# Performance work log

Measured on AMD Instinct MI355X. Metric: run time of the kernel, lower is better.

The kernel has to match this reference:

```python
import jax, jax.numpy as jnp
import numpy as np


def _shift(x, k):
    # roll time axis forward by k, zero-filling the first k steps
    if k == 0:
        return x
    return jnp.pad(x, ((0, 0), (k, 0), (0, 0)))[:, : x.shape[1]]


def _stu_conv(u, v, n):
    # u: (B,L,D), v: (L,K) spectral filters; non-tensordot branch of conv()
    B, L, D = u.shape
    K = v.shape[1]
    sgn = jnp.where(jnp.arange(L) % 2 == 1, -1.0, 1.0).astype(jnp.float32)[None, :, None, None]
    ue = jnp.broadcast_to(u[:, :, None, :], (B, L, K, D)).astype(jnp.float32)
    U = jnp.stack([ue, ue * sgn], axis=-1)                     # (B,L,K,D,2)
    Uf = jnp.fft.rfft(U, n=n, axis=1)
    vf = jnp.fft.rfft(v.astype(jnp.float32)[None, :, :, None, None], n=n, axis=1)
    Uc = jnp.fft.irfft(vf * Uf, n=n, axis=1)[:, :L]            # (B,L,K,D,2)
    U_plus = Uc[..., 0]
    U_minus = Uc[..., 1] * sgn
    return U_plus.astype(u.dtype), U_minus.astype(u.dtype)


def setup_inputs() -> dict:
    key = jax.random.key(0)
    ks = jax.random.split(key, 6)
    B, L, D, K, k_u, k_y = 2, 1024, 512, 16, 3, 2
    u = jax.random.normal(ks[0], (B, L, D), jnp.float32)
    filters = jax.random.normal(ks[1], (L, K), jnp.float32) / np.float32(np.sqrt(L))
    M_u = jax.random.normal(ks[2], (D, k_u, D), jnp.float32) * 0.01
    M_y = jax.random.normal(ks[3], (D, k_y, D), jnp.float32) * 0.01
    M_phi_plus = jax.random.normal(ks[4], (K, D, D), jnp.float32) * 0.01
    M_phi_minus = jax.random.normal(ks[5], (K, D, D), jnp.float32) * 0.01
    return {"u": u, "filters": filters, "M_u": M_u, "M_y": M_y,
            "M_phi_plus": M_phi_plus, "M_phi_minus": M_phi_minus}


def reference(u, filters, M_u, M_y, M_phi_plus, M_phi_minus):
    B, L, D = u.shape
    n = 1 << int(np.ceil(np.log2(2 * L - 1)))  # nearest power of two >= 2L-1
    k_u = M_u.shape[1]
    k_y = M_y.shape[1]

    # FFT-based long convolution with the +/- sign trick
    U_plus, U_minus = _stu_conv(u, filters, n)
    spectral = (jnp.einsum('blkd,kdo->blo', U_plus, M_phi_plus)
                + jnp.einsum('blkd,kdo->blo', U_minus, M_phi_minus))

    # input-AR term of compute_ar_strict: sum_j u[t+1-j] @ M_u[:, j-1].T (shifts 0..k_u-1)
    u_sh = jnp.stack([_shift(u, j - 1) for j in range(1, k_u + 1)], axis=1)  # (B,k_u,L,D)
    y_in = jnp.einsum('bjlf,ijf->bli', u_sh, M_u)

    z = spectral + y_in  # (B,L,D)

    # output-AR recurrence of compute_ar_strict as a scan
    def step(y_buf, z_t):
        y_t = z_t + jnp.einsum('bjf,djf->bd', y_buf, M_y)
        y_buf = jnp.concatenate([y_t[:, None], y_buf[:, :-1]], axis=1)
        return y_buf, y_t

    _, ys = jax.lax.scan(step, jnp.zeros((B, k_y, D), z.dtype), jnp.swapaxes(z, 0, 1))
    return jnp.swapaxes(ys, 0, 1)  # (B,L,D)
```

## Files before the change

### kernel.cpp

```cpp
#include <hip/hip_runtime.h>
#include <hip/hip_bf16.h>


using bf16 = __hip_bfloat16;
typedef __attribute__((ext_vector_type(8))) short bf16x8;
typedef __attribute__((ext_vector_type(4))) float f32x4;

#define B_   2
#define L_   1024
#define D_   512
#define K_   16
#define KT   17920
#define ROWS 2048
#define NTAP 6
#define PBLD 3584
#define SPLITD 14
#define SPLITR 6
#define ZBROWS 1032
#define NKS 40
#define NTD 20

#define WAIT_VM6 0x0F76
#define WAIT_VM4 0x0F74
#define WAIT_VM0 0x0F70

__device__ __forceinline__ void gll16(const void* g, void* l) {
    __builtin_amdgcn_global_load_lds(
        (const __attribute__((address_space(1))) unsigned int*)g,
        (__attribute__((address_space(3))) unsigned int*)l, 16, 0, 0);
}

__global__ void prep_all(const float* __restrict__ u, const float* __restrict__ fil,
                         const float* __restrict__ Mu, const float* __restrict__ My,
                         const float* __restrict__ Mp, const float* __restrict__ Mm,
                         bf16* __restrict__ U, bf16* __restrict__ BT,
                         bf16* __restrict__ PB, bf16* __restrict__ W,
                         bf16* __restrict__ Myb, bf16* __restrict__ BTT,
                         bf16* __restrict__ uPT) {
    __shared__ bf16 t[64][72];
    int bid = blockIdx.x, tid = threadIdx.x;
    auto pack4 = [](float4 v) {
        ushort4 o; bf16 h;
        h = __float2bfloat16(v.x); o.x = *(unsigned short*)&h;
        h = __float2bfloat16(v.y); o.y = *(unsigned short*)&h;
        h = __float2bfloat16(v.z); o.z = *(unsigned short*)&h;
        h = __float2bfloat16(v.w); o.w = *(unsigned short*)&h;
        return o;
    };
    if (bid < 3072) {
        int e4 = bid * 256 + tid;
        int r = e4 / 384, rem = e4 % 384;
        int tt = rem >> 7, f = (rem & 127) * 4;
        int b = r >> 10, l = r & 1023;
        float4 v = {0.f, 0.f, 0.f, 0.f};
        if (l >= tt) v = *(const float4*)&u[((size_t)b * L_ + l - tt) * D_ + f];
        *(ushort4*)&U[(size_t)r * KT + 16384 + tt * 512 + f] = pack4(v);
    } else if (bid < 3840) {
        int e4 = (bid - 3072) * 256 + tid;
        int o = e4 / 384, tf4 = (e4 % 384) * 4;
        float4 v = *(const float4*)&Mu[(size_t)o * 1536 + tf4];
        *(ushort4*)&BT[(size_t)o * KT + 16384 + tf4] = pack4(v);
    } else if (bid < 4352) {
        int e4 = (bid - 3840) * 256 + tid;
        int n = e4 >> 8, c4 = (e4 & 255) * 4;
        float4 v;
        if (c4 < 512) {
            v.x = (n == c4) ? 1.f : 0.f;     v.y = (n == c4 + 1) ? 1.f : 0.f;
            v.z = (n == c4 + 2) ? 1.f : 0.f; v.w = (n == c4 + 3) ? 1.f : 0.f;
        } else v = *(const float4*)&My[(size_t)n * 1024 + (c4 - 512)];
        *(ushort4*)&PB[(size_t)n * PBLD + c4] = pack4(v);
    } else if (bid < 5120) {
        int tile = bid - 4352;
        int set = tile >> 8, rem = tile & 255;
        int k = rem >> 4, g = (rem >> 2) & 3, kb = rem & 3;
        for (int idx = tid; idx < 4096; idx += 256) {
            int i = idx >> 5, jp = idx & 31;
            int j = ((jp >> 3) ^ ((i >> 1) & 3)) * 8 + (jp & 7);
            int x = g * 128 + i - kb * 32 - j - (set == 2 ? 1 : 0);
            float v = 0.f;
            if (x >= 0) {
                int row = (set == 0) ? 2 * x : 2 * x + 1;
                v = fil[row * K_ + k];
            }
            W[(size_t)tile * 4096 + idx] = __float2bfloat16(v);
        }
    } else if (bid < 5632) {
        int e4 = (bid - 5120) * 256 + tid;
        float4 v = *(const float4*)&My[(size_t)e4 * 4];
        *(ushort4*)&Myb[(size_t)e4 * 4] = pack4(v);
    } else {
        int tt = bid - 5632;
        int zb = tt >> 6, rem = tt & 63;
        int bx = rem & 7, by = rem >> 3;
        int col = tid & 63, r0 = (tid >> 6) * 16;
        if (zb < 32) {
            int dt = bx * 64, ot = by * 64, c = zb;
            int k = c & 15;
            const float* sp = Mp + (size_t)k * D_ * D_;
            const float* sm = Mm + (size_t)k * D_ * D_;
            float sg = (c < 16) ? 1.f : -1.f;
            for (int i = 0; i < 16; ++i) {
                size_t o_ = (size_t)(dt + r0 + i) * D_ + ot + col;
                t[r0 + i][col] = __float2bfloat16(sp[o_] + sg * sm[o_]);
            }
            __syncthreads();
            for (int i = 0; i < 16; ++i)
                BT[(size_t)(ot + r0 + i) * KT + c * D_ + dt + col] = t[col][r0 + i];
        } else if (zb < 34) {
            int h = zb - 32;
            int dt = bx * 64, ft = by * 64;
            for (int i = 0; i < 16; ++i)
                t[r0 + i][col] = __float2bfloat16(My[(size_t)(dt + r0 + i) * 1024 + (1 - h) * 512 + ft + col]);
            __syncthreads();
            for (int i = 0; i < 16; ++i)
                BTT[(size_t)(ft + r0 + i) * 1024 + h * 512 + dt + col] = t[col][r0 + i];
        } else {
            for (int it = 0; it < 4; ++it) {
                int b = it >> 1, p = it & 1;
                int mt = bx * 64, dt = by * 64;
                __syncthreads();
                for (int i = 0; i < 16; ++i)
                    t[r0 + i][col] = __float2bfloat16(u[((size_t)b * L_ + 2 * (mt + r0 + i) + p) * D_ + dt + col]);
                __syncthreads();
                for (int i = 0; i < 16; ++i)
                    uPT[((size_t)it * 512 + dt + r0 + i) * 512 + mt + col] = t[col][r0 + i];
            }
        }
    }
}

__device__ __forceinline__ void phi_body(
    const bf16* A, int lda, const bf16* BT, int ldb,
    bf16* out, int ldo, int klen, const bf16* add, int lad,
    int row0, int col0, bf16* sA, bf16* sB)
{
    const int tid = threadIdx.x, lane = tid & 63, wave = tid >> 6;
    const int wm = (wave & 1) * 64, wn = (wave >> 1) * 64;
    const int ml = lane & 15, q = lane >> 4;
    const int srow = lane >> 2, scol = (((lane & 3) ^ ((srow >> 1) & 3))) * 8;
    const int swz = ((ml >> 1) & 3);
    f32x4 acc[4][4] = {};

    for (int k = 0; k < klen; k += 32) {
        __syncthreads();
        #pragma unroll
        for (int repi = 0; repi < 2; ++repi) {
            int a = wave + repi * 4;
            gll16(A  + (size_t)(row0 + a * 16 + srow) * lda + k + scol, &sA[a * 512]);
            gll16(BT + (size_t)(col0 + a * 16 + srow) * ldb + k + scol, &sB[a * 512]);
        }
        __syncthreads();
        bf16x8 af[4], bfr[4];
        #pragma unroll
        for (int i = 0; i < 4; ++i)
            af[i] = *(const bf16x8*)&sA[(wm + i * 16 + ml) * 32 + (q ^ swz) * 8];
        #pragma unroll
        for (int j = 0; j < 4; ++j)
            bfr[j] = *(const bf16x8*)&sB[(wn + j * 16 + ml) * 32 + (q ^ swz) * 8];
        #pragma unroll
        for (int i = 0; i < 4; ++i)
            #pragma unroll
            for (int j = 0; j < 4; ++j)
                acc[i][j] = __builtin_amdgcn_mfma_f32_16x16x32_bf16(af[i], bfr[j], acc[i][j], 0, 0, 0);
    }
    #pragma unroll
    for (int i = 0; i < 4; ++i)
        #pragma unroll
        for (int j = 0; j < 4; ++j)
            #pragma unroll
            for (int reg = 0; reg < 4; ++reg) {
                int r = row0 + wm + i * 16 + q * 4 + reg;
                int cc = col0 + wn + j * 16 + ml;
                float v = acc[i][j][reg];
                if (add) v += __bfloat162float(add[(size_t)r * lad + cc]);
                out[(size_t)r * ldo + cc] = __float2bfloat16(v);
            }
}

__global__ void k_ztaps(const bf16* __restrict__ partD, float* __restrict__ z,
                        bf16* __restrict__ zbuf, bf16* PB, const bf16* BTT) {
    __shared__ bf16 sA[4096];
    __shared__ bf16 sB[4096];
    int bid = blockIdx.x;
    if (bid < 32) {
        int row0 = (bid & 3) * 128, col0 = (bid >> 2) * 128;
        phi_body(PB + 3 * 512, PBLD, BTT, 1024, PB + 5 * 512, PBLD, 1024,
                 nullptr, 0, row0, col0, sA, sB);
        return;
    }
    if (bid == 32) {
        ushort4 z4 = {0, 0, 0, 0};
        for (int i = 0; i < 8; ++i) {
            int e4 = i * 256 + threadIdx.x;
            int b = e4 >> 10, rem = e4 & 1023;
            int g = rem >> 7, c4 = (rem & 127) * 4;
            *(ushort4*)&zbuf[(size_t)(b * ZBROWS + g) * 512 + c4] = z4;
        }
        return;
    }
    int t = (bid - 33) * 256 + threadIdx.x;
    int r = t >> 7, f4 = (t & 127) * 4;
    const ushort4* p = (const ushort4*)partD;
    float4 s = {0.f, 0.f, 0.f, 0.f};
    #pragma unroll
    for (int c = 0; c < SPLITD; ++c) {
        ushort4 v = p[(size_t)c * (ROWS * D_ / 4) + t];
        s.x += __uint_as_float((unsigned)v.x << 16);
        s.y += __uint_as_float((unsigned)v.y << 16);
        s.z += __uint_as_float((unsigned)v.z << 16);
        s.w += __uint_as_float((unsigned)v.w << 16);
    }
    ((float4*)z)[t] = s;
    ushort4 zb4;
    { bf16 h;
      h = __float2bfloat16(s.x); zb4.x = *(unsigned short*)&h;
      h = __float2bfloat16(s.y); zb4.y = *(unsigned short*)&h;
      h = __float2bfloat16(s.z); zb4.z = *(unsigned short*)&h;
      h = __float2bfloat16(s.w); zb4.w = *(unsigned short*)&h; }
    int b = r >> 10, li = r & 1023;
    *(ushort4*)&zbuf[(size_t)(b * ZBROWS + 8 + li) * 512 + f4] = zb4;
}

__global__ void reduce_out(const float* __restrict__ z, const bf16* __restrict__ partR,
                           float* __restrict__ out) {
    int t = blockIdx.x * 256 + threadIdx.x;
    if (t >= ROWS * D_ / 4) return;
    float4 s = ((const float4*)z)[t];
    const ushort4* p = (const ushort4*)partR;
    #pragma unroll
    for (int c = 0; c < SPLITR; ++c) {
        ushort4 v = p[(size_t)c * (ROWS * D_ / 4) + t];
        s.x += __uint_as_float((unsigned)v.x << 16);
        s.y += __uint_as_float((unsigned)v.y << 16);
        s.z += __uint_as_float((unsigned)v.z << 16);
        s.w += __uint_as_float((unsigned)v.w << 16);
    }
    ((float4*)out)[t] = s;
}

__global__ __launch_bounds__(256, 3) void conv_misc(
    const bf16* __restrict__ W, const bf16* __restrict__ uPT,
    bf16* __restrict__ U,
    const bf16* PB, const bf16* BTT, const bf16* Myb)
{
    __shared__ bf16 sA[3][4096];
    __shared__ bf16 sB[3][4096];
    const int z = blockIdx.z;
    if (z < 3) {
        int row0 = blockIdx.x * 128, col0 = blockIdx.y * 128;
        bf16* BTTw = (bf16*)BTT; bf16* PBw = (bf16*)PB;
        if (z == 0)
            phi_body(PB, PBLD, BTT, 1024, PBw + 2 * 512, PBLD, 1024,
                     nullptr, 0, row0, col0, &sA[0][0], &sB[0][0]);
        else if (z == 1)
            phi_body(BTT + 512, 1024, Myb + 512, 1024,
                     BTTw + (size_t)512 * 1024, 1024, 512,
                     nullptr, 0, row0, col0, &sA[0][0], &sB[0][0]);
        else
            phi_body(BTT + 512, 1024, Myb, 1024,
                     BTTw + (size_t)512 * 1024 + 512, 1024, 512,
                     BTT, 1024, row0, col0, &sA[0][0], &sB[0][0]);
        return;
    }
    const int zc = z - 3;
    const int mt = 3 - blockIdx.x, dt = blockIdx.y * 128;
    const int t = zc & 3, b = (zc >> 2) & 1, k = zc >> 3;
    const int pb_ = t & 1;
    const int p = (t & 1) ^ (t >> 1);
    const int set = (t < 2) ? 0 : (t == 2 ? 1 : 2);
    const int ch = (t < 2) ? k : 16 + k;
    const int plane = b * 2 + pb_;
    const int tid = threadIdx.x, lane = tid & 63, wave = tid >> 6;
    const int wm = (wave & 1) * 64, wn = (wave >> 1) * 64;
    const int ml = lane & 15, q = lane >> 4;
    const int srow = lane >> 2, scol = (((lane & 3) ^ ((srow >> 1) & 3))) * 8;
    const int swz = ((ml >> 1) & 3);
    f32x4 acc[4][4] = {};
    const int n = (mt + 1) * 4;

    const bf16* bB0 = uPT + ((size_t)plane * 512 + dt + wave * 16       + srow) * 512 + scol;
    const bf16* bB1 = uPT + ((size_t)plane * 512 + dt + (wave + 4) * 16 + srow) * 512 + scol;
    const bf16* wbase = W + ((size_t)(set * 16 + k) * 16) * 4096;
    auto stage = [&](int s, int buf) {
        const bf16* wt = wbase + ((size_t)((mt - (s >> 2)) * 4 + (s & 3))) * 4096;
        gll16(wt + wave * 512 + lane * 8, &sA[buf][wave * 512]);
        gll16(wt + (wave + 4) * 512 + lane * 8, &sA[buf][(wave + 4) * 512]);
        gll16(bB0 + s * 32, &sB[buf][wave * 512]);
        gll16(bB1 + s * 32, &sB[buf][(wave + 4) * 512]);
    };
    auto compute = [&](int c) {
        bf16x8 af[4], bfr[4];
        #pragma unroll
        for (int i = 0; i < 4; ++i)
            af[i] = *(const bf16x8*)&sA[c][(wm + i * 16 + ml) * 32 + (q ^ swz) * 8];
        #pragma unroll
        for (int j = 0; j < 4; ++j)
            bfr[j] = *(const bf16x8*)&sB[c][(wn + j * 16 + ml) * 32 + (q ^ swz) * 8];
        #pragma unroll
        for (int i = 0; i < 4; ++i)
            #pragma unroll
            for (int j = 0; j < 4; ++j)
                acc[i][j] = __builtin_amdgcn_mfma_f32_16x16x32_bf16(af[i], bfr[j], acc[i][j], 0, 0, 0);
    };
    stage(0, 0); stage(1, 1);
    int c = 0, nb = 2;
    for (int i = 0; i < n - 1; ++i) {
        __builtin_amdgcn_s_waitcnt(WAIT_VM4);
        __builtin_amdgcn_s_barrier();
        if (i + 2 < n) stage(i + 2, nb);
        compute(c);
        c = (c == 2) ? 0 : c + 1; nb = (nb == 2) ? 0 : nb + 1;
    }
    __builtin_amdgcn_s_waitcnt(WAIT_VM0);
    __builtin_amdgcn_s_barrier();
    compute(c);

    #pragma unroll
    for (int i = 0; i < 4; ++i)
        #pragma unroll
        for (int j = 0; j < 4; ++j)
            #pragma unroll
            for (int reg = 0; reg < 4; ++reg) {
                int m = mt * 128 + wm + i * 16 + q * 4 + reg;
                int l = 2 * m + p;
                int d = dt + wn + j * 16 + ml;
                U[(size_t)(b * L_ + l) * KT + ch * 512 + d] = __float2bfloat16(acc[i][j][reg]);
            }
}

__global__ __launch_bounds__(512, 2) void gemm_d(
    const bf16* __restrict__ U, const bf16* __restrict__ BT,
    bf16* __restrict__ part, const bf16* PB, const bf16* BTT)
{
    __shared__ bf16 sA[4][8192];
    __shared__ bf16 sB[4][8192];
    int id = blockIdx.x;
    const int tid = threadIdx.x, lane = tid & 63, wave = tid >> 6;
    if (id < 32) {
        if (wave >= 4) {
            for (int i = 0; i < 64; ++i) __syncthreads();
            return;
        }
        int r0_ = (id & 3) * 128, c0_ = (id >> 2) * 128;
        phi_body(PB + 512, PBLD, BTT, 1024, (bf16*)PB + 3 * 512, PBLD, 1024,
                 nullptr, 0, r0_, c0_, &sA[0][0], &sB[0][0]);
        return;
    }
    id -= 32;
    const int zz = id >> 4;
    const int n_ = id & 15;
    const int row0 = (n_ >> 1) * 256, col0 = (n_ & 1) * 256;
    const int k0 = zz * (KT / SPLITD);

    const int wm = (wave >> 2) * 128;
    const int wn = (wave & 3) * 64;
    const int ml = lane & 15, q16 = lane >> 4;
    const int srow = lane >> 2, scol = (((lane & 3) ^ ((srow >> 1) & 3))) * 8;
    const int swz = ((ml >> 1) & 3);
    const int koff = (q16 ^ swz) * 8;

    const int a0 = 2 * wave, a1 = 2 * wave + 1;
    const bf16* bA0 = U  + (size_t)(row0 + a0 * 16 + srow) * KT + k0 + scol;
    const bf16* bA1 = U  + (size_t)(row0 + a1 * 16 + srow) * KT + k0 + scol;
    const bf16* bB0 = BT + (size_t)(col0 + a0 * 16 + srow) * KT + k0 + scol;
    const bf16* bB1 = BT + (size_t)(col0 + a1 * 16 + srow) * KT + k0 + scol;
    auto stageA = [&](int s) {
        if (s >= NKS) return;
        gll16(bA0 + s * 32, &sA[s & 3][a0 * 512]);
        gll16(bA1 + s * 32, &sA[s & 3][a1 * 512]);
    };
    auto stageB = [&](int s) {
        if (s >= NKS) return;
        gll16(bB0 + s * 32, &sB[s & 3][a0 * 512]);
        gll16(bB1 + s * 32, &sB[s & 3][a1 * 512]);
    };

    f32x4 acc[8][4] = {};

    stageB(0); stageB(1); stageA(0); stageA(1);
    stageB(2); stageB(3); stageA(2);
    __builtin_amdgcn_s_waitcnt(WAIT_VM6);
    __builtin_amdgcn_s_barrier();

    for (int t = 0; t < NTD; ++t) {
        const int u0 = (2 * t) & 3, u1 = u0 + 1;
        bf16x8 bfr[4][2];
        #pragma unroll
        for (int ph = 0; ph < 4; ++ph) {
            bf16x8 af[2][2];
            if (ph == 0) {
                #pragma unroll
                for (int fc = 0; fc < 4; ++fc) {
                    bfr[fc][0] = *(const bf16x8*)&sB[u0][(wn + fc * 16 + ml) * 32 + koff];
                    bfr[fc][1] = *(const bf16x8*)&sB[u1][(wn + fc * 16 + ml) * 32 + koff];
                }
            }
            #pragma unroll
            for (int f2 = 0; f2 < 2; ++f2) {
                int R = wm + (2 * ph + f2) * 16 + ml;
                af[f2][0] = *(const bf16x8*)&sA[u0][R * 32 + koff];
                af[f2][1] = *(const bf16x8*)&sA[u1][R * 32 + koff];
            }
            if (ph == 0)      stageA(2 * t + 3);
            else if (ph == 1) stageB(2 * t + 4);
            else if (ph == 2) stageB(2 * t + 5);
            else              stageA(2 * t + 4);
            __builtin_amdgcn_s_barrier();
            __builtin_amdgcn_s_setprio(1);
            #pragma unroll
            for (int f2 = 0; f2 < 2; ++f2)
                #pragma unroll
                for (int fc = 0; fc < 4; ++fc) {
                    acc[2 * ph + f2][fc] = __builtin_amdgcn_mfma_f32_16x16x32_bf16(
                        af[f2][0], bfr[fc][0], acc[2 * ph + f2][fc], 0, 0, 0);
                    acc[2 * ph + f2][fc] = __builtin_amdgcn_mfma_f32_16x16x32_bf16(
                        af[f2][1], bfr[fc][1], acc[2 * ph + f2][fc], 0, 0, 0);
                }
            __builtin_amdgcn_s_setprio(0);
            if (ph == 3) {
                if (t < NTD - 2)       __builtin_amdgcn_s_waitcnt(WAIT_VM6);
                else if (t == NTD - 2) __builtin_amdgcn_s_waitcnt(WAIT_VM0);
            }
            __builtin_amdgcn_s_barrier();
        }
    }

    bf16* o = part + (size_t)zz * ROWS * D_;
    #pragma unroll
    for (int i = 0; i < 8; ++i)
        #pragma unroll
        for (int j = 0; j < 4; ++j)
            #pragma unroll
            for (int reg = 0; reg < 4; ++reg) {
                int r = row0 + wm + i * 16 + q16 * 4 + reg;
                int cc = col0 + wn + j * 16 + ml;
                o[(size_t)r * D_ + cc] = __float2bfloat16(acc[i][j][reg]);
            }
}

__device__ __forceinline__ void mm128_pair(
    const bf16* Abase, int alda, const bf16* Bbase, int ldb, int n,
    bf16* o, int row0, int col0, bf16 (*sA)[4096], bf16 (*sB)[4096])
{
    const int tid = threadIdx.x, lane = tid & 63, wave = tid >> 6;
    const int wm = (wave & 1) * 64, wn = (wave >> 1) * 64;
    const int ml = lane & 15, q = lane >> 4;
    const int srow = lane >> 2, scol = (((lane & 3) ^ ((srow >> 1) & 3))) * 8;
    const int swz = ((ml >> 1) & 3);
    f32x4 acc[4][4] = {};

    const bf16* bA0 = Abase + (size_t)(wave * 16 + srow) * alda + scol;
    const bf16* bA1 = Abase + (size_t)((wave + 4) * 16 + srow) * alda + scol;
    const bf16* bB0 = Bbase + (size_t)(wave * 16 + srow) * ldb + scol;
    const bf16* bB1 = Bbase + (size_t)((wave + 4) * 16 + srow) * ldb + scol;
    auto stage = [&](int s) {
        int buf = s & 3;
        gll16(bA0 + s * 32, &sA[buf][wave * 512]);
        gll16(bA1 + s * 32, &sA[buf][(wave + 4) * 512]);
        gll16(bB0 + s * 32, &sB[buf][wave * 512]);
        gll16(bB1 + s * 32, &sB[buf][(wave + 4) * 512]);
    };
    auto compute = [&](int c) {
        bf16x8 af[4], bfr[4];
        #pragma unroll
        for (int i = 0; i < 4; ++i)
            af[i] = *(const bf16x8*)&sA[c][(wm + i * 16 + ml) * 32 + (q ^ swz) * 8];
        #pragma unroll
        for (int j = 0; j < 4; ++j)
            bfr[j] = *(const bf16x8*)&sB[c][(wn + j * 16 + ml) * 32 + (q ^ swz) * 8];
        #pragma unroll
        for (int i = 0; i < 4; ++i)
            #pragma unroll
            for (int j = 0; j < 4; ++j)
                acc[i][j] = __builtin_amdgcn_mfma_f32_16x16x32_bf16(af[i], bfr[j], acc[i][j], 0, 0, 0);
    };
    stage(0); stage(1);
    const int npair = n >> 1;
    for (int p = 0; p < npair; ++p) {
        __builtin_amdgcn_s_waitcnt(WAIT_VM0);
        __builtin_amdgcn_s_barrier();
        if (2 * p + 2 < n) { stage(2 * p + 2); stage(2 * p + 3); }
        compute((2 * p) & 3);
        compute((2 * p + 1) & 3);
    }
    #pragma unroll
    for (int i = 0; i < 4; ++i)
        #pragma unroll
        for (int j = 0; j < 4; ++j)
            #pragma unroll
            for (int reg = 0; reg < 4; ++reg) {
                int r = row0 + wm + i * 16 + q * 4 + reg;
                int cc = col0 + wn + j * 16 + ml;
                o[(size_t)r * D_ + cc] = __float2bfloat16(acc[i][j][reg]);
            }
}

__global__ __launch_bounds__(256, 2) void gemm_r(
    const bf16* __restrict__ zbuf, const bf16* __restrict__ BT,
    bf16* __restrict__ part)
{
    __shared__ bf16 sA[4][4096];
    __shared__ bf16 sB[4][4096];
    const int row0 = blockIdx.x * 128, col0 = blockIdx.y * 128;
    const int zz = blockIdx.z;
    const int s = 1 + zz;
    const int b = row0 >> 10, li0 = row0 & 1023;
    mm128_pair(zbuf + ((size_t)(b * ZBROWS + 8 + li0 - s)) * 512, 512,
               BT + (size_t)col0 * PBLD + (size_t)zz * 512, PBLD,
               16, part + (size_t)zz * ROWS * D_, row0, col0, sA, sB);
}

extern "C" void kernel_launch(void* const* d_in, const int* in_sizes, int n_in,
                              void* d_out, int out_size, void* d_ws, size_t ws_size,
                              hipStream_t stream) {
    const float* u   = (const float*)d_in[0];
    const float* fil = (const float*)d_in[1];
    const float* Mu  = (const float*)d_in[2];
    const float* My  = (const float*)d_in[3];
    const float* Mp  = (const float*)d_in[4];
    const float* Mm  = (const float*)d_in[5];
    float* out = (float*)d_out;

    char* ws = (char*)d_ws;
    size_t off = 0;
    auto alloc = [&](size_t bytes) { void* p = ws + off; off = (off + bytes + 255) & ~(size_t)255; return p; };
    bf16*  U    = (bf16*) alloc((size_t)ROWS * KT * 2);
    bf16*  BT   = (bf16*) alloc((size_t)512 * KT * 2);
    bf16*  PB   = (bf16*) alloc((size_t)512 * PBLD * 2);
    bf16*  BTT  = (bf16*) alloc((size_t)1024 * 1024 * 2);
    bf16*  Myb  = (bf16*) alloc((size_t)512 * 1024 * 2);
    float* z    = (float*)alloc((size_t)ROWS * D_ * 4);
    bf16*  zb   = (bf16*) alloc((size_t)B_ * ZBROWS * 512 * 2);
    char*  region = (char*)alloc((size_t)16 * ROWS * D_ * 2);
    bf16*  W    = (bf16*)region;
    bf16*  uPT  = (bf16*)(region + (size_t)768 * 4096 * 2);
    bf16*  partD = (bf16*)region;
    bf16*  partR = (bf16*)region;

    prep_all<<<7872, 256, 0, stream>>>(u, fil, Mu, My, Mp, Mm,
                                       U, BT, PB, W, Myb, BTT, uPT);

    conv_misc<<<dim3(4, 4, 131), 256, 0, stream>>>(W, uPT, U, PB, BTT, Myb);

    gemm_d<<<256, 512, 0, stream>>>(U, BT, partD, PB, BTT);

    k_ztaps<<<1057, 256, 0, stream>>>(partD, z, zb, PB, BTT);

    gemm_r<<<dim3(16, 4, SPLITR), 256, 0, stream>>>(zb, PB + 512, partR);

    reduce_out<<<(ROWS * D_ / 4 + 255) / 256, 256, 0, stream>>>(z, partR, out);
}
```

Baseline: 228.8 us.

## Retile Toeplitz conv GEMM to 256x256 eight-wave blocks with 4-stage pipeline

Replaces the 128x128 four-wave conv_misc kernel with conv8, which uses 512-thread blocks computing 256x256 output tiles through a 4-deep LDS ring. Loads are interleaved across MFMA phases and MFMA sections run at raised priority. Causal zero tiles are now read from a zeroed region written by an extra prep block, so every block runs a uniform k-loop and avoids branching. The phi GEMMs are moved to an 8-wave variant. The larger tiles aim to raise data reuse per load and MFMA utilisation, at the cost of fewer blocks, more registers, and some wasted MFMA work on zero tiles.

```diff
diff --git a/kernel.cpp b/kernel.cpp
--- a/kernel.cpp
+++ b/kernel.cpp
@@ -19,6 +19,7 @@
 #define ZBROWS 1032
 #define NKS 40
 #define NTD 20
+#define WZOFF 4194304
 
 #define WAIT_VM6 0x0F76
 #define WAIT_VM4 0x0F74
@@ -88,7 +89,7 @@
         int e4 = (bid - 5120) * 256 + tid;
         float4 v = *(const float4*)&My[(size_t)e4 * 4];
         *(ushort4*)&Myb[(size_t)e4 * 4] = pack4(v);
-    } else {
+    } else if (bid < 7872) {
         int tt = bid - 5632;
         int zb = tt >> 6, rem = tt & 63;
         int bx = rem & 7, by = rem >> 3;
@@ -126,6 +127,10 @@
                     uPT[((size_t)it * 512 + dt + r0 + i) * 512 + mt + col] = t[col][r0 + i];
             }
         }
+    } else {
+        ushort4 z4 = {0, 0, 0, 0};
+        for (int i = 0; i < 4; ++i)
+            *(ushort4*)&W[(size_t)WZOFF + (size_t)(i * 256 + tid) * 4] = z4;
     }
 }
 
@@ -149,6 +154,51 @@
             gll16(A  + (size_t)(row0 + a * 16 + srow) * lda + k + scol, &sA[a * 512]);
             gll16(BT + (size_t)(col0 + a * 16 + srow) * ldb + k + scol, &sB[a * 512]);
         }
+        __syncthreads();
+        bf16x8 af[4], bfr[4];
+        #pragma unroll
+        for (int i = 0; i < 4; ++i)
+            af[i] = *(const bf16x8*)&sA[(wm + i * 16 + ml) * 32 + (q ^ swz) * 8];
+        #pragma unroll
+        for (int j = 0; j < 4; ++j)
+            bfr[j] = *(const bf16x8*)&sB[(wn + j * 16 + ml) * 32 + (q ^ swz) * 8];
+        #pragma unroll
+        for (int i = 0; i < 4; ++i)
+            #pragma unroll
+            for (int j = 0; j < 4; ++j)
+                acc[i][j] = __builtin_amdgcn_mfma_f32_16x16x32_bf16(af[i], bfr[j], acc[i][j], 0, 0, 0);
+    }
+    #pragma unroll
+    for (int i = 0; i < 4; ++i)
+        #pragma unroll
+        for (int j = 0; j < 4; ++j)
+            #pragma unroll
+            for (int reg = 0; reg < 4; ++reg) {
+                int r = row0 + wm + i * 16 + q * 4 + reg;
+                int cc = col0 + wn + j * 16 + ml;
+                float v = acc[i][j][reg];
+                if (add) v += __bfloat162float(add[(size_t)r * lad + cc]);
+                out[(size_t)r * ldo + cc] = __float2bfloat16(v);
+            }
+}
+
+__device__ __forceinline__ void phi_body8(
+    const bf16* A, int lda, const bf16* BT, int ldb,
+    bf16* out, int ldo, int klen, const bf16* add, int lad,
+    int row0, int col0, bf16* sA, bf16* sB)
+{
+    const int tid = threadIdx.x, lane = tid & 63, wave = tid >> 6;
+    const int wm = (wave & 1) * 64, wn = (wave >> 1) * 64;
+    const int ml = lane & 15, q = lane >> 4;
+    const int srow = lane >> 2, scol = (((lane & 3) ^ ((srow >> 1) & 3))) * 8;
+    const int swz = ((ml >> 1) & 3);
+    f32x4 acc[4][4] = {};
+
+    for (int k = 0; k < klen; k += 32) {
+        __syncthreads();
+        gll16(A  + (size_t)(row0 + wave * 16 + srow) * lda + k + scol, &sA[wave * 512]);
+        gll16(BT + (size_t)(col0 + (2 * wave) * 16 + srow) * ldb + k + scol, &sB[(2 * wave) * 512]);
+        gll16(BT + (size_t)(col0 + (2 * wave + 1) * 16 + srow) * ldb + k + scol, &sB[(2 * wave + 1) * 512]);
         __syncthreads();
         bf16x8 af[4], bfr[4];
         #pragma unroll
@@ -238,92 +288,132 @@
     ((float4*)out)[t] = s;
 }
 
-__global__ __launch_bounds__(256, 3) void conv_misc(
+__global__ __launch_bounds__(512, 2) void conv8(
     const bf16* __restrict__ W, const bf16* __restrict__ uPT,
     bf16* __restrict__ U,
     const bf16* PB, const bf16* BTT, const bf16* Myb)
 {
-    __shared__ bf16 sA[3][4096];
-    __shared__ bf16 sB[3][4096];
-    const int z = blockIdx.z;
-    if (z < 3) {
-        int row0 = blockIdx.x * 128, col0 = blockIdx.y * 128;
+    __shared__ bf16 sA[4][8192];
+    __shared__ bf16 sB[4][8192];
+    int id = blockIdx.x;
+    const int tid = threadIdx.x, lane = tid & 63, wave = tid >> 6;
+    if (id < 24) {
+        int pz = id >> 3, sub = id & 7;
+        int row0 = (sub & 3) * 128, col0 = (sub >> 2) * 256;
         bf16* BTTw = (bf16*)BTT; bf16* PBw = (bf16*)PB;
-        if (z == 0)
-            phi_body(PB, PBLD, BTT, 1024, PBw + 2 * 512, PBLD, 1024,
-                     nullptr, 0, row0, col0, &sA[0][0], &sB[0][0]);
-        else if (z == 1)
-            phi_body(BTT + 512, 1024, Myb + 512, 1024,
-                     BTTw + (size_t)512 * 1024, 1024, 512,
-                     nullptr, 0, row0, col0, &sA[0][0], &sB[0][0]);
+        if (pz == 0)
+            phi_body8(PB, PBLD, BTT, 1024, PBw + 2 * 512, PBLD, 1024,
+                      nullptr, 0, row0, col0, &sA[0][0], &sB[0][0]);
+        else if (pz == 1)
+            phi_body8(BTT + 512, 1024, Myb + 512, 1024,
+                      BTTw + (size_t)512 * 1024, 1024, 512,
+                      nullptr, 0, row0, col0, &sA[0][0], &sB[0][0]);
         else
-            phi_body(BTT + 512, 1024, Myb, 1024,
-                     BTTw + (size_t)512 * 1024 + 512, 1024, 512,
-                     BTT, 1024, row0, col0, &sA[0][0], &sB[0][0]);
+            phi_body8(BTT + 512, 1024, Myb, 1024,
+                      BTTw + (size_t)512 * 1024 + 512, 1024, 512,
+                      BTT, 1024, row0, col0, &sA[0][0], &sB[0][0]);
         return;
     }
-    const int zc = z - 3;
-    const int mt = 3 - blockIdx.x, dt = blockIdx.y * 128;
-    const int t = zc & 3, b = (zc >> 2) & 1, k = zc >> 3;
-    const int pb_ = t & 1;
-    const int p = (t & 1) ^ (t >> 1);
-    const int set = (t < 2) ? 0 : (t == 2 ? 1 : 2);
-    const int ch = (t < 2) ? k : 16 + k;
+    const int cid = id - 24;
+    const int mt2 = (cid < 256) ? 1 : 0;
+    const int zc = (cid & 255) >> 1;
+    const int dt2 = cid & 1;
+    const int pc = zc & 3, b = (zc >> 2) & 1, k = zc >> 3;
+    const int pb_ = pc & 1;
+    const int p = (pc & 1) ^ (pc >> 1);
+    const int set = (pc < 2) ? 0 : (pc == 2 ? 1 : 2);
+    const int ch = (pc < 2) ? k : 16 + k;
     const int plane = b * 2 + pb_;
-    const int tid = threadIdx.x, lane = tid & 63, wave = tid >> 6;
-    const int wm = (wave & 1) * 64, wn = (wave >> 1) * 64;
-    const int ml = lane & 15, q = lane >> 4;
+    const int nks = (mt2 + 1) * 8;
+    const int NT = nks >> 1;
+
+    const int wm = (wave >> 2) * 128;
+    const int wn = (wave & 3) * 64;
+    const int ml = lane & 15, q16 = lane >> 4;
     const int srow = lane >> 2, scol = (((lane & 3) ^ ((srow >> 1) & 3))) * 8;
     const int swz = ((ml >> 1) & 3);
-    f32x4 acc[4][4] = {};
-    const int n = (mt + 1) * 4;
-
-    const bf16* bB0 = uPT + ((size_t)plane * 512 + dt + wave * 16       + srow) * 512 + scol;
-    const bf16* bB1 = uPT + ((size_t)plane * 512 + dt + (wave + 4) * 16 + srow) * 512 + scol;
+    const int koff = (q16 ^ swz) * 8;
+
+    const int a0 = 2 * wave, a1 = a0 + 1;
+    const int rb = mt2 * 2 + (a0 >> 3);
     const bf16* wbase = W + ((size_t)(set * 16 + k) * 16) * 4096;
-    auto stage = [&](int s, int buf) {
-        const bf16* wt = wbase + ((size_t)((mt - (s >> 2)) * 4 + (s & 3))) * 4096;
-        gll16(wt + wave * 512 + lane * 8, &sA[buf][wave * 512]);
-        gll16(wt + (wave + 4) * 512 + lane * 8, &sA[buf][(wave + 4) * 512]);
-        gll16(bB0 + s * 32, &sB[buf][wave * 512]);
-        gll16(bB1 + s * 32, &sB[buf][(wave + 4) * 512]);
+    const bf16* wzero = W + (size_t)WZOFF;
+    const bf16* bB0 = uPT + ((size_t)plane * 512 + dt2 * 256 + a0 * 16 + srow) * 512 + scol;
+    const bf16* bB1 = uPT + ((size_t)plane * 512 + dt2 * 256 + a1 * 16 + srow) * 512 + scol;
+
+    auto stageA = [&](int s) {
+        if (s >= nks) return;
+        int s4 = s >> 2;
+        const bf16* t0 = (rb >= s4)
+            ? wbase + (size_t)((rb - s4) * 4 + (s & 3)) * 4096 : wzero;
+        gll16(t0 + ((a0 & 7) * 512 + lane * 8), &sA[s & 3][a0 * 512]);
+        gll16(t0 + ((a1 & 7) * 512 + lane * 8), &sA[s & 3][a1 * 512]);
     };
-    auto compute = [&](int c) {
-        bf16x8 af[4], bfr[4];
-        #pragma unroll
-        for (int i = 0; i < 4; ++i)
-            af[i] = *(const bf16x8*)&sA[c][(wm + i * 16 + ml) * 32 + (q ^ swz) * 8];
-        #pragma unroll
-        for (int j = 0; j < 4; ++j)
-            bfr[j] = *(const bf16x8*)&sB[c][(wn + j * 16 + ml) * 32 + (q ^ swz) * 8];
-        #pragma unroll
-        for (int i = 0; i < 4; ++i)
-            #pragma unroll
-            for (int j = 0; j < 4; ++j)
-                acc[i][j] = __builtin_amdgcn_mfma_f32_16x16x32_bf16(af[i], bfr[j], acc[i][j], 0, 0, 0);
+    auto stageB = [&](int s) {
+        if (s >= nks) return;
+        gll16(bB0 + s * 32, &sB[s & 3][a0 * 512]);
+        gll16(bB1 + s * 32, &sB[s & 3][a1 * 512]);
     };
-    stage(0, 0); stage(1, 1);
-    int c = 0, nb = 2;
-    for (int i = 0; i < n - 1; ++i) {
-        __builtin_amdgcn_s_waitcnt(WAIT_VM4);
-        __builtin_amdgcn_s_barrier();
-        if (i + 2 < n) stage(i + 2, nb);
-        compute(c);
-        c = (c == 2) ? 0 : c + 1; nb = (nb == 2) ? 0 : nb + 1;
-    }
-    __builtin_amdgcn_s_waitcnt(WAIT_VM0);
+
+    f32x4 acc[8][4] = {};
+
+    stageB(0); stageB(1); stageA(0); stageA(1);
+    stageB(2); stageB(3); stageA(2);
+    __builtin_amdgcn_s_waitcnt(WAIT_VM6);
     __builtin_amdgcn_s_barrier();
-    compute(c);
+
+    for (int t = 0; t < NT; ++t) {
+        const int u0 = (2 * t) & 3, u1 = u0 + 1;
+        bf16x8 bfr[4][2];
+        #pragma unroll
+        for (int ph = 0; ph < 4; ++ph) {
+            bf16x8 af[2][2];
+            if (ph == 0) {
+                #pragma unroll
+                for (int fc = 0; fc < 4; ++fc) {
+                    bfr[fc][0] = *(const bf16x8*)&sB[u0][(wn + fc * 16 + ml) * 32 + koff];
+                    bfr[fc][1] = *(const bf16x8*)&sB[u1][(wn + fc * 16 + ml) * 32 + koff];
+                }
+            }
+            #pragma unroll
+            for (int f2 = 0; f2 < 2; ++f2) {
+                int R = wm + (2 * ph + f2) * 16 + ml;
+                af[f2][0] = *(const bf16x8*)&sA[u0][R * 32 + koff];
+                af[f2][1] = *(const bf16x8*)&sA[u1][R * 32 + koff];
+            }
+            if (ph == 0)      stageA(2 * t + 3);
+            else if (ph == 1) stageB(2 * t + 4);
+            else if (ph == 2) stageB(2 * t + 5);
+            else              stageA(2 * t + 4);
+            __builtin_amdgcn_s_barrier();
+            __builtin_amdgcn_s_setprio(1);
+            #pragma unroll
+            for (int f2 = 0; f2 < 2; ++f2)
+                #pragma unroll
+                for (int fc = 0; fc < 4; ++fc) {
+                    acc[2 * ph + f2][fc] = __builtin_amdgcn_mfma_f32_16x16x32_bf16(
+                        af[f2][0], bfr[fc][0], acc[2 * ph + f2][fc], 0, 0, 0);
+                    acc[2 * ph + f2][fc] = __builtin_amdgcn_mfma_f32_16x16x32_bf16(
+                        af[f2][1], bfr[fc][1], acc[2 * ph + f2][fc], 0, 0, 0);
+                }
+            __builtin_amdgcn_s_setprio(0);
+            if (ph == 3) {
+                if (t < NT - 2)       __builtin_amdgcn_s_waitcnt(WAIT_VM6);
+                else if (t == NT - 2) __builtin_amdgcn_s_waitcnt(WAIT_VM0);
+            }
+            __builtin_amdgcn_s_barrier();
+        }
+    }
 
     #pragma unroll
-    for (int i = 0; i < 4; ++i)
+    for (int i = 0; i < 8; ++i)
         #pragma unroll
         for (int j = 0; j < 4; ++j)
             #pragma unroll
             for (int reg = 0; reg < 4; ++reg) {
-                int m = mt * 128 + wm + i * 16 + q * 4 + reg;
+                int m = mt2 * 256 + wm + i * 16 + q16 * 4 + reg;
                 int l = 2 * m + p;
-                int d = dt + wn + j * 16 + ml;
+                int d = dt2 * 256 + wn + j * 16 + ml;
                 U[(size_t)(b * L_ + l) * KT + ch * 512 + d] = __float2bfloat16(acc[i][j][reg]);
             }
 }
@@ -537,10 +627,10 @@
     bf16*  partD = (bf16*)region;
     bf16*  partR = (bf16*)region;
 
-    prep_all<<<7872, 256, 0, stream>>>(u, fil, Mu, My, Mp, Mm,
+    prep_all<<<7873, 256, 0, stream>>>(u, fil, Mu, My, Mp, Mm,
                                        U, BT, PB, W, Myb, BTT, uPT);
 
-    conv_misc<<<dim3(4, 4, 131), 256, 0, stream>>>(W, uPT, U, PB, BTT, Myb);
+    conv8<<<536, 512, 0, stream>>>(W, uPT, U, PB, BTT, Myb);
 
     gemm_d<<<256, 512, 0, stream>>>(U, BT, partD, PB, BTT);
 
```

Result: no change. 231.7 us (+1.3%).
